# Performance work log

Hardware: AMD Instinct MI355X
Metric: run time of the kernel (lower is better)

Reference implementation:

```python
import jax, jax.numpy as jnp
import numpy as np

EPS = 1e-5

def _conv1x1(x, w, b):
    # x: [B, Cin, L], w: [Cout, Cin], b: [Cout]
    return jnp.einsum('oc,bcl->bol', w, x) + b[None, :, None]

def _bn(x, g, b):
    # BatchNorm1d in training mode: batch stats over (B, L), biased variance
    m = jnp.mean(x, axis=(0, 2), keepdims=True)
    v = jnp.var(x, axis=(0, 2), keepdims=True)
    return g[None, :, None] * (x - m) * jax.lax.rsqrt(v + EPS) + b[None, :, None]

def setup_inputs() -> dict:
    key = jax.random.key(0)
    ks = jax.random.split(key, 16)
    B, H, L, K = 32, 32, 32768, 7
    rel, im, out = H // 16, H // 8, H // 4          # 2, 4, 8
    cat = (1 + K) * rel                              # 16
    w = lambda k, shape: jax.random.normal(k, shape, jnp.float32) * 0.1
    return {
        'x': jax.random.normal(ks[0], (B, H, L), jnp.float32),
        'w_phi': w(ks[1], (rel, H)),  'b_phi': w(ks[2], (rel,)),
        'w_psi': w(ks[3], (rel, H)),  'b_psi': w(ks[4], (rel,)),
        'w_beta': w(ks[5], (out, H)), 'b_beta': w(ks[6], (out,)),
        'w_cw1': w(ks[7], (im, cat)), 'b_cw1': w(ks[8], (im,)),
        'w_cw2': w(ks[9], (out, im)), 'b_cw2': w(ks[10], (out,)),
        'w_out': w(ks[11], (H, out)), 'b_out': w(ks[12], (H,)),
        'g_cat': jnp.ones((cat,), jnp.float32),  'be_cat': jnp.zeros((cat,), jnp.float32),
        'g_im': jnp.ones((im,), jnp.float32),    'be_im': jnp.zeros((im,), jnp.float32),
        'g_aggr': jnp.ones((out,), jnp.float32), 'be_aggr': jnp.zeros((out,), jnp.float32),
        'g_hid': jnp.ones((H,), jnp.float32),    'be_hid': jnp.zeros((H,), jnp.float32),
        'kernel_size': 7,
    }

def reference(x, w_phi, b_phi, w_psi, b_psi, w_beta, b_beta,
              w_cw1, b_cw1, w_cw2, b_cw2, w_out, b_out,
              g_cat, be_cat, g_im, be_im, g_aggr, be_aggr, g_hid, be_hid,
              kernel_size):
    B, H, L = x.shape
    phi = _conv1x1(x, w_phi, b_phi)                       # [B, rel, L]
    psi = _conv1x1(x, w_psi, b_psi)                       # [B, rel, L]
    p = kernel_size // 2
    psi_pad = jnp.pad(psi, ((0, 0), (0, 0), (p, p)))
    # F.unfold with kernel (k,1): channel index = c*k + j -> stack kernel axis after channel
    psi_unf = jnp.stack([psi_pad[:, :, j:j + L] for j in range(kernel_size)], axis=2)
    psi_unf = psi_unf.reshape(B, psi.shape[1] * kernel_size, L)   # [B, rel*k, L]
    h = jnp.concatenate([phi, psi_unf], axis=1)           # [B, (1+k)*rel, L]
    h = jax.nn.relu(_bn(h, g_cat, be_cat))
    h = _conv1x1(h, w_cw1, b_cw1)
    h = jax.nn.relu(_bn(h, g_im, be_im))
    weight = _conv1x1(h, w_cw2, b_cw2)                    # [B, out, L]
    beta = _conv1x1(x, w_beta, b_beta)                    # [B, out, L]
    aggr = jax.nn.relu(_bn(weight * beta, g_aggr, be_aggr))
    y = x + _conv1x1(aggr, w_out, b_out)
    return jax.nn.relu(_bn(y, g_hid, be_hid))
```

## Files before the change

### kernel.cpp

```cpp
#include <hip/hip_runtime.h>
#include <math.h>

#define Bn 32
#define Hc 32
#define Ln 32768
#define RELC 2
#define IMC 4
#define OC 8
#define CATC 16
#define KS 7
#define NPOS (Bn*Ln)
#define TPB 256
#define VPT 4
#define PPB (TPB*VPT)
#define TILES (Ln/PPB)
#define NBLK (Bn*TILES)
#define NSLOT 16
#define SSTR 128

#define iS_PHI  0
#define iSS_PHI 2
#define iS_PSI  4
#define iSS_PSI 6
#define iS_T    8
#define iSS_T   12
#define iS_AP   16
#define iSS_AP  24
#define iS_Y    32
#define iSS_Y   64
#define bPF  0
#define bPFS 6
#define bQL  12
#define bQLS 18
#define NBST 24

#define FMA4(A,S,V) { A.x=fmaf((S),(V).x,A.x); A.y=fmaf((S),(V).y,A.y); A.z=fmaf((S),(V).z,A.z); A.w=fmaf((S),(V).w,A.w); }

__device__ inline float4 affrelu(float4 v, float a, float d){
    float4 r;
    r.x=fmaxf(fmaf(a,v.x,d),0.f); r.y=fmaxf(fmaf(a,v.y,d),0.f);
    r.z=fmaxf(fmaf(a,v.z,d),0.f); r.w=fmaxf(fmaf(a,v.w,d),0.f);
    return r;
}
__device__ inline double wredd(double v){
    #pragma unroll
    for (int o=32;o>0;o>>=1) v += __shfl_down(v,o,64);
    return v;
}
__device__ inline float wredf(float v){
    #pragma unroll
    for (int o=32;o>0;o>>=1) v += __shfl_down(v,o,64);
    return v;
}
__device__ inline void atomAddD(double* p, double v){ unsafeAtomicAdd(p, v); }

__device__ inline unsigned short f2b(float f){
    unsigned int u = __float_as_uint(f);
    u += 0x7FFFu + ((u>>16)&1u);
    return (unsigned short)(u>>16);
}
__device__ inline float b2f(unsigned short h){ return __uint_as_float(((unsigned int)h)<<16); }
__device__ inline ushort4 pack4r(float4 v, float4* r){
    ushort4 h;
    h.x=f2b(v.x); h.y=f2b(v.y); h.z=f2b(v.z); h.w=f2b(v.w);
    r->x=b2f(h.x); r->y=b2f(h.y); r->z=b2f(h.z); r->w=b2f(h.w);
    return h;
}
__device__ inline ushort4 pack4(float4 v){
    ushort4 h;
    h.x=f2b(v.x); h.y=f2b(v.y); h.z=f2b(v.z); h.w=f2b(v.w);
    return h;
}
__device__ inline float4 unpack4(ushort4 h){
    return make_float4(b2f(h.x),b2f(h.y),b2f(h.z),b2f(h.w));
}
typedef unsigned short us8 __attribute__((ext_vector_type(8)));
typedef float f4nt __attribute__((ext_vector_type(4)));
__device__ inline void ntstore4(float* p, float4 v){
    union { float4 a; f4nt b; } u; u.a = v;
    __builtin_nontemporal_store(u.b, (f4nt*)p);
}

template<int NCH>
__device__ void affines(const double* __restrict__ stats, const double* __restrict__ bstats,
                        const float* g_cat, const float* be_cat,
                        const float* g_im,  const float* be_im,
                        const float* g_ag,  const float* be_ag,
                        const float* g_hid, const float* be_hid,
                        double (*redS)[16], double (*redQ)[16],
                        double* bstL, float* aAll, float* dAll, int tid)
{
    if (tid < NBST) bstL[tid] = bstats[tid];
    for (int p = tid; p < NCH*16; p += TPB){
        int ch = p >> 4, s = p & 15;
        int si, qi;
        if (ch < 2)       { si = iS_PHI+ch;           qi = iSS_PHI+ch; }
        else if (ch < 16) { int cp=(ch-2)/KS;         si = iS_PSI+cp;  qi = iSS_PSI+cp; }
        else if (ch < 20) { int i=ch-16;              si = iS_T+i;     qi = iSS_T+i; }
        else if (ch < 28) { int o=ch-20;              si = iS_AP+o;    qi = iSS_AP+o; }
        else              { int h=ch-28;              si = iS_Y+h;     qi = iSS_Y+h; }
        redS[ch][s] = stats[(size_t)s*SSTR + si];
        redQ[ch][s] = stats[(size_t)s*SSTR + qi];
    }
    __syncthreads();
    if (tid < NCH){
        double S=0, SS=0;
        #pragma unroll
        for (int s=0;s<16;++s){ S += redS[tid][s]; SS += redQ[tid][s]; }
        float g, be;
        if (tid < 16){
            if (tid >= 2){
                int cp=(tid-2)/KS, j=(tid-2)%KS, d=j-KS/2;
                if (d>0) for (int i=0;i<d;++i)   { S-=bstL[bPF+cp*3+i]; SS-=bstL[bPFS+cp*3+i]; }
                if (d<0) for (int i=3+d;i<3;++i) { S-=bstL[bQL+cp*3+i]; SS-=bstL[bQLS+cp*3+i]; }
            }
            g=g_cat[tid]; be=be_cat[tid];
        } else if (tid < 20){ g=g_im[tid-16]; be=be_im[tid-16]; }
        else if (tid < 28){ g=g_ag[tid-20]; be=be_ag[tid-20]; }
        else { g=g_hid[tid-28]; be=be_hid[tid-28]; }
        const double N=(double)NPOS;
        double m=S/N, v=SS/N-m*m, inv=1.0/sqrt(v+1e-5);
        aAll[tid]=(float)(g*inv);
        dAll[tid]=be-(float)(m*inv*g);
    }
}

__global__ void __launch_bounds__(TPB) k1m(
    const float* __restrict__ x,
    const float* __restrict__ w_phi, const float* __restrict__ b_phi,
    const float* __restrict__ w_psi, const float* __restrict__ b_psi,
    const float* __restrict__ w_beta,const float* __restrict__ b_beta,
    unsigned short* __restrict__ phiB, unsigned short* __restrict__ psiB,
    unsigned short* __restrict__ betaB, unsigned short* __restrict__ xB,
    double* __restrict__ stats, double* __restrict__ bstats)
{
    __shared__ __align__(16) float wl[Hc*12 + 12];
    __shared__ double rbuf[4][8];
    const int tid = threadIdx.x;
    for (int i = tid; i < Hc*12; i += TPB) {
        int h = i/12, j = i%12;
        float v;
        if (j < 2)      v = w_phi[j*Hc + h];
        else if (j < 4) v = w_psi[(j-2)*Hc + h];
        else            v = w_beta[(j-4)*Hc + h];
        wl[h*12 + j] = v;
    }
    if (tid < 12)
        wl[Hc*12+tid] = (tid<2) ? b_phi[tid] : (tid<4) ? b_psi[tid-2] : b_beta[tid-4];
    __syncthreads();

    const int b    = blockIdx.x / TILES;
    const int tile = blockIdx.x % TILES;
    const int l0   = tile*PPB + tid*VPT;
    double* st = stats + (size_t)(blockIdx.x & (NSLOT-1))*SSTR;

    const float* xp = x + (size_t)b*Hc*Ln + l0;
    unsigned short* xw = xB + (size_t)b*Hc*Ln + l0;

    float4 accA[4];
    #pragma unroll
    for (int j=0;j<4;++j){ float bb = wl[Hc*12+j]; accA[j]=make_float4(bb,bb,bb,bb); }
    #pragma unroll 8
    for (int h=0; h<Hc; ++h) {
        const float4 xv = *(const float4*)(xp + (size_t)h*Ln);
        const float4 w0 = *(const float4*)(&wl[h*12+0]);
        FMA4(accA[0],w0.x,xv); FMA4(accA[1],w0.y,xv);
        FMA4(accA[2],w0.z,xv); FMA4(accA[3],w0.w,xv);
        *(ushort4*)(xw + (size_t)h*Ln) = pack4(xv);
    }
    float4 accB[OC];
    #pragma unroll
    for (int o=0;o<OC;++o){ float bb = wl[Hc*12+4+o]; accB[o]=make_float4(bb,bb,bb,bb); }
    #pragma unroll 8
    for (int h=0; h<Hc; ++h) {
        const float4 hv = unpack4(*(const ushort4*)(xw + (size_t)h*Ln));
        const float4 w1 = *(const float4*)(&wl[h*12+4]);
        const float4 w2 = *(const float4*)(&wl[h*12+8]);
        FMA4(accB[0],w1.x,hv); FMA4(accB[1],w1.y,hv); FMA4(accB[2],w1.z,hv); FMA4(accB[3],w1.w,hv);
        FMA4(accB[4],w2.x,hv); FMA4(accB[5],w2.y,hv); FMA4(accB[6],w2.z,hv); FMA4(accB[7],w2.w,hv);
    }

    float4 rphi[2], rpsi[2];
    #pragma unroll
    for (int c=0;c<RELC;++c){
        ushort4 hp = pack4r(accA[c], &rphi[c]);
        *(ushort4*)(phiB + ((size_t)(b*RELC+c))*Ln + l0) = hp;
        ushort4 hq = pack4r(accA[2+c], &rpsi[c]);
        *(ushort4*)(psiB + ((size_t)(b*RELC+c))*Ln + l0) = hq;
    }
    #pragma unroll
    for (int o=0;o<OC;++o)
        *(ushort4*)(betaB + ((size_t)(b*OC+o))*Ln + l0) = pack4(accB[o]);

    double vals[8];
    #pragma unroll
    for (int c=0;c<2;++c){
        float4 v = rphi[c];
        vals[c]   = (double)v.x+v.y+v.z+v.w;
        vals[2+c] = (double)v.x*v.x+(double)v.y*v.y+(double)v.z*v.z+(double)v.w*v.w;
        float4 u = rpsi[c];
        vals[4+c] = (double)u.x+u.y+u.z+u.w;
        vals[6+c] = (double)u.x*u.x+(double)u.y*u.y+(double)u.z*u.z+(double)u.w*u.w;
    }
    if (tile==0 || tile==TILES-1) {
        #pragma unroll
        for (int c=0;c<2;++c){
            const float pv[4] = {rpsi[c].x, rpsi[c].y, rpsi[c].z, rpsi[c].w};
            #pragma unroll
            for (int e=0;e<4;++e){
                int le = l0+e;
                if (le < 3) {
                    atomAddD(&bstats[bPF +c*3+le], (double)pv[e]);
                    atomAddD(&bstats[bPFS+c*3+le], (double)pv[e]*pv[e]);
                }
                if (le >= Ln-3) {
                    int i = le-(Ln-3);
                    atomAddD(&bstats[bQL +c*3+i], (double)pv[e]);
                    atomAddD(&bstats[bQLS+c*3+i], (double)pv[e]*pv[e]);
                }
            }
        }
    }
    const int lane=tid&63, wid=tid>>6;
    #pragma unroll
    for (int i=0;i<8;++i){ double r=wredd(vals[i]); if(lane==0) rbuf[wid][i]=r; }
    __syncthreads();
    if (tid<8) atomAddD(&st[iS_PHI+tid], rbuf[0][tid]+rbuf[1][tid]+rbuf[2][tid]+rbuf[3][tid]);
}

#define STAGE_PSI_V(psiT)                                                                  \
    {                                                                                      \
        int c_ = tid >> 7, k_ = tid & 127;                                                 \
        us8 v_ = *(const us8*)(psiB + ((size_t)(b*RELC+c_))*Ln + lb + 8*k_);               \
        _Pragma("unroll")                                                                  \
        for (int j_=0;j_<8;++j_) psiT[c_][3+8*k_+j_] = b2f(v_[j_]);                        \
        if (tid < 6){ int cc=tid/3, ii=tid%3;                                              \
            psiT[cc][ii] = (tile>0) ? b2f(psiB[((size_t)(b*RELC+cc))*Ln + lb-3+ii]) : 0.f; }\
        else if (tid < 12){ int kk=tid-6, cc=kk/3, ii=kk%3;                                \
            psiT[cc][1027+ii] = (tile<TILES-1) ? b2f(psiB[((size_t)(b*RELC+cc))*Ln + lb+1024+ii]) : 0.f; } \
    }

#define COMPUTE_T(tacc,aCat,dCat,w1s,b1s,psiT)                                             \
    _Pragma("unroll")                                                                      \
    for (int o=0;o<IMC;++o){ float bb=b1s[o]; tacc[o]=make_float4(bb,bb,bb,bb); }          \
    _Pragma("unroll")                                                                      \
    for (int c=0;c<RELC;++c){                                                              \
        float4 pv = unpack4(*(const ushort4*)(phiB + ((size_t)(b*RELC+c))*Ln + lb + li));  \
        float4 hv = affrelu(pv, aCat[c], dCat[c]);                                         \
        _Pragma("unroll")                                                                  \
        for (int o=0;o<IMC;++o) FMA4(tacc[o], w1s[o*CATC+c], hv);                          \
    }                                                                                      \
    _Pragma("unroll")                                                                      \
    for (int c=0;c<RELC;++c){                                                              \
        float4 A  = *(const float4*)&psiT[c][li];                                          \
        float4 Bv = *(const float4*)&psiT[c][li+4];                                        \
        float4 Cv = *(const float4*)&psiT[c][li+8];                                        \
        float pr[12] = {A.x,A.y,A.z,A.w, Bv.x,Bv.y,Bv.z,Bv.w, Cv.x,Cv.y,Cv.z,Cv.w};        \
        _Pragma("unroll")                                                                  \
        for (int j=0;j<KS;++j){                                                            \
            int ch = 2 + c*KS + j;                                                         \
            float a=aCat[ch], d=dCat[ch];                                                  \
            float4 hv;                                                                     \
            hv.x=fmaxf(fmaf(a,pr[j+0],d),0.f);                                             \
            hv.y=fmaxf(fmaf(a,pr[j+1],d),0.f);                                             \
            hv.z=fmaxf(fmaf(a,pr[j+2],d),0.f);                                             \
            hv.w=fmaxf(fmaf(a,pr[j+3],d),0.f);                                             \
            _Pragma("unroll")                                                              \
            for (int o=0;o<IMC;++o) FMA4(tacc[o], w1s[o*CATC+ch], hv);                     \
        }                                                                                  \
    }

#define COMPUTE_AG(ag,tacc,aIm,dIm,aAg,dAg,w2s,b2s)                                        \
    {                                                                                      \
        float4 h2[IMC];                                                                    \
        _Pragma("unroll")                                                                  \
        for (int i=0;i<IMC;++i) h2[i]=affrelu(tacc[i],aIm[i],dIm[i]);                      \
        _Pragma("unroll")                                                                  \
        for (int o=0;o<OC;++o){                                                            \
            float bb=b2s[o];                                                               \
            float4 w=make_float4(bb,bb,bb,bb);                                             \
            _Pragma("unroll")                                                              \
            for (int i=0;i<IMC;++i) FMA4(w,w2s[o*IMC+i],h2[i]);                            \
            float4 bv = unpack4(*(const ushort4*)(betaB + ((size_t)(b*OC+o))*Ln + lb + li)); \
            float4 av; av.x=w.x*bv.x; av.y=w.y*bv.y; av.z=w.z*bv.z; av.w=w.w*bv.w;         \
            ag[o]=affrelu(av, aAg[o], dAg[o]);                                             \
        }                                                                                  \
    }

__global__ void __launch_bounds__(TPB) k3t(
    const unsigned short* __restrict__ phiB, const unsigned short* __restrict__ psiB,
    const float* __restrict__ w_cw1, const float* __restrict__ b_cw1,
    const float* __restrict__ g_cat, const float* __restrict__ be_cat,
    double* __restrict__ stats, const double* __restrict__ bstats)
{
    __shared__ float w1s[IMC*CATC], b1s[IMC];
    __shared__ __align__(16) float psiT[2][1032];
    __shared__ double rbuf[4][8];
    __shared__ double redS[16][16], redQ[16][16];
    __shared__ double bstL[NBST];
    __shared__ float aAll[16], dAll[16];
    const int tid = threadIdx.x;
    const int b    = blockIdx.x / TILES;
    const int tile = blockIdx.x % TILES;
    const int lb   = tile*PPB;
    const int li   = tid*VPT;
    double* st = stats + (size_t)(blockIdx.x & (NSLOT-1))*SSTR;

    if (tid < IMC*CATC) w1s[tid] = w_cw1[tid];
    if (tid < IMC)      b1s[tid] = b_cw1[tid];
    STAGE_PSI_V(psiT)
    affines<16>(stats,bstats, g_cat,be_cat, 0,0, 0,0, 0,0, redS,redQ,bstL,aAll,dAll, tid);
    __syncthreads();

    float4 tacc[IMC];
    COMPUTE_T(tacc,aAll,dAll,w1s,b1s,psiT)

    double vals[8];
    #pragma unroll
    for (int o=0;o<IMC;++o){
        float4 v = tacc[o];
        vals[o]   = (double)v.x+v.y+v.z+v.w;
        vals[4+o] = (double)v.x*v.x+(double)v.y*v.y+(double)v.z*v.z+(double)v.w*v.w;
    }
    const int lane=tid&63, wid=tid>>6;
    #pragma unroll
    for (int i=0;i<8;++i){ double r=wredd(vals[i]); if(lane==0) rbuf[wid][i]=r; }
    __syncthreads();
    if (tid<8) atomAddD(&st[iS_T+tid], rbuf[0][tid]+rbuf[1][tid]+rbuf[2][tid]+rbuf[3][tid]);
}

__global__ void __launch_bounds__(TPB) k5a(
    const unsigned short* __restrict__ phiB, const unsigned short* __restrict__ psiB,
    const unsigned short* __restrict__ betaB,
    const float* __restrict__ w_cw1, const float* __restrict__ b_cw1,
    const float* __restrict__ w_cw2, const float* __restrict__ b_cw2,
    const float* __restrict__ g_cat, const float* __restrict__ be_cat,
    const float* __restrict__ g_im,  const float* __restrict__ be_im,
    double* __restrict__ stats, const double* __restrict__ bstats)
{
    __shared__ float w1s[IMC*CATC], b1s[IMC], w2s[OC*IMC], b2s[OC];
    __shared__ __align__(16) float psiT[2][1032];
    __shared__ double rbuf[4][16];
    __shared__ double redS[20][16], redQ[20][16];
    __shared__ double bstL[NBST];
    __shared__ float aAll[20], dAll[20];
    const int tid = threadIdx.x;
    const int b    = blockIdx.x / TILES;
    const int tile = blockIdx.x % TILES;
    const int lb   = tile*PPB;
    const int li   = tid*VPT;
    double* st = stats + (size_t)(blockIdx.x & (NSLOT-1))*SSTR;

    if (tid < IMC*CATC) w1s[tid] = w_cw1[tid];
    if (tid < IMC)      b1s[tid] = b_cw1[tid];
    if (tid>=64 && tid<64+OC*IMC) w2s[tid-64]=w_cw2[tid-64];
    if (tid>=96 && tid<96+OC)     b2s[tid-96]=b_cw2[tid-96];
    STAGE_PSI_V(psiT)
    affines<20>(stats,bstats, g_cat,be_cat, g_im,be_im, 0,0, 0,0, redS,redQ,bstL,aAll,dAll, tid);
    __syncthreads();

    float4 tacc[IMC];
    COMPUTE_T(tacc,aAll,dAll,w1s,b1s,psiT)

    double vals[16];
    {
        float4 h2[IMC];
        #pragma unroll
        for (int i=0;i<IMC;++i) h2[i]=affrelu(tacc[i],aAll[16+i],dAll[16+i]);
        #pragma unroll
        for (int o=0;o<OC;++o){
            float bb=b2s[o];
            float4 w=make_float4(bb,bb,bb,bb);
            #pragma unroll
            for (int i=0;i<IMC;++i) FMA4(w,w2s[o*IMC+i],h2[i]);
            float4 bv = unpack4(*(const ushort4*)(betaB + ((size_t)(b*OC+o))*Ln + lb + li));
            float4 av; av.x=w.x*bv.x; av.y=w.y*bv.y; av.z=w.z*bv.z; av.w=w.w*bv.w;
            vals[o]   = (double)av.x+av.y+av.z+av.w;
            vals[8+o] = (double)av.x*av.x+(double)av.y*av.y+(double)av.z*av.z+(double)av.w*av.w;
        }
    }
    const int lane=tid&63, wid=tid>>6;
    #pragma unroll
    for (int i=0;i<16;++i){ double r=wredd(vals[i]); if(lane==0) rbuf[wid][i]=r; }
    __syncthreads();
    if (tid<16) atomAddD(&st[iS_AP+tid], rbuf[0][tid]+rbuf[1][tid]+rbuf[2][tid]+rbuf[3][tid]);
}

__global__ void __launch_bounds__(TPB) k7y(
    const unsigned short* __restrict__ xB,
    const unsigned short* __restrict__ phiB, const unsigned short* __restrict__ psiB,
    const unsigned short* __restrict__ betaB,
    const float* __restrict__ w_cw1, const float* __restrict__ b_cw1,
    const float* __restrict__ w_cw2, const float* __restrict__ b_cw2,
    const float* __restrict__ w_out, const float* __restrict__ b_out,
    const float* __restrict__ g_cat, const float* __restrict__ be_cat,
    const float* __restrict__ g_im,  const float* __restrict__ be_im,
    const float* __restrict__ g_ag,  const float* __restrict__ be_ag,
    double* __restrict__ stats, const double* __restrict__ bstats)
{
    __shared__ float w1s[IMC*CATC], b1s[IMC], w2s[OC*IMC], b2s[OC];
    __shared__ __align__(16) float wos[Hc*OC];
    __shared__ float bos[Hc];
    __shared__ __align__(16) float psiT[2][1032];
    __shared__ float fredS[Hc][4], fredQ[Hc][4];
    __shared__ double redS[28][16], redQ[28][16];
    __shared__ double bstL[NBST];
    __shared__ float aAll[28], dAll[28];
    const int tid = threadIdx.x;
    const int b    = blockIdx.x / TILES;
    const int tile = blockIdx.x % TILES;
    const int lb   = tile*PPB;
    const int li   = tid*VPT;
    double* st = stats + (size_t)(blockIdx.x & (NSLOT-1))*SSTR;

    if (tid < IMC*CATC) w1s[tid] = w_cw1[tid];
    if (tid < IMC)      b1s[tid] = b_cw1[tid];
    if (tid>=64 && tid<64+OC*IMC) w2s[tid-64]=w_cw2[tid-64];
    if (tid>=96 && tid<96+OC)     b2s[tid-96]=b_cw2[tid-96];
    wos[tid] = w_out[tid];
    if (tid>=128 && tid<128+Hc) bos[tid-128]=b_out[tid-128];
    STAGE_PSI_V(psiT)
    affines<28>(stats,bstats, g_cat,be_cat, g_im,be_im, g_ag,be_ag, 0,0,
                redS,redQ,bstL,aAll,dAll, tid);
    __syncthreads();

    float4 tacc[IMC];
    COMPUTE_T(tacc,aAll,dAll,w1s,b1s,psiT)
    float4 ag[OC];
    COMPUTE_AG(ag,tacc,(aAll+16),(dAll+16),(aAll+20),(dAll+20),w2s,b2s)

    const int lane=tid&63, wid=tid>>6;
    const unsigned short* xb = xB + (size_t)b*Hc*Ln + lb + li;
    #pragma unroll 8
    for (int h=0;h<Hc;++h){
        float4 y = unpack4(*(const ushort4*)(xb + (size_t)h*Ln));
        float bb=bos[h]; y.x+=bb; y.y+=bb; y.z+=bb; y.w+=bb;
        #pragma unroll
        for (int o=0;o<OC;++o) FMA4(y, wos[h*OC+o], ag[o]);
        float fs=y.x+y.y+y.z+y.w;
        float fq=y.x*y.x+y.y*y.y+y.z*y.z+y.w*y.w;
        fs=wredf(fs); fq=wredf(fq);
        if (lane==0){ fredS[h][wid]=fs; fredQ[h][wid]=fq; }
    }
    __syncthreads();
    if (tid<Hc){
        double s=(double)fredS[tid][0]+fredS[tid][1]+fredS[tid][2]+fredS[tid][3];
        double q=(double)fredQ[tid][0]+fredQ[tid][1]+fredQ[tid][2]+fredQ[tid][3];
        atomAddD(&st[iS_Y +tid], s);
        atomAddD(&st[iSS_Y+tid], q);
    }
}

__global__ void __launch_bounds__(TPB) k9o(
    const unsigned short* __restrict__ xB,
    const unsigned short* __restrict__ phiB, const unsigned short* __restrict__ psiB,
    const unsigned short* __restrict__ betaB,
    const float* __restrict__ w_cw1, const float* __restrict__ b_cw1,
    const float* __restrict__ w_cw2, const float* __restrict__ b_cw2,
    const float* __restrict__ w_out, const float* __restrict__ b_out,
    const float* __restrict__ g_cat, const float* __restrict__ be_cat,
    const float* __restrict__ g_im,  const float* __restrict__ be_im,
    const float* __restrict__ g_ag,  const float* __restrict__ be_ag,
    const float* __restrict__ g_hid, const float* __restrict__ be_hid,
    float* __restrict__ out,
    const double* __restrict__ stats, const double* __restrict__ bstats)
{
    __shared__ float w1s[IMC*CATC], b1s[IMC], w2s[OC*IMC], b2s[OC];
    __shared__ __align__(16) float wos[Hc*OC];
    __shared__ float bos[Hc];
    __shared__ __align__(16) float psiT[2][1032];
    __shared__ double redS[60][16], redQ[60][16];
    __shared__ double bstL[NBST];
    __shared__ float aAll[60], dAll[60];
    const int tid = threadIdx.x;
    const int b    = blockIdx.x / TILES;
    const int tile = blockIdx.x % TILES;
    const int lb   = tile*PPB;
    const int li   = tid*VPT;

    if (tid < IMC*CATC) w1s[tid] = w_cw1[tid];
    if (tid < IMC)      b1s[tid] = b_cw1[tid];
    if (tid>=64 && tid<64+OC*IMC) w2s[tid-64]=w_cw2[tid-64];
    if (tid>=96 && tid<96+OC)     b2s[tid-96]=b_cw2[tid-96];
    wos[tid] = w_out[tid];
    if (tid>=128 && tid<128+Hc) bos[tid-128]=b_out[tid-128];
    STAGE_PSI_V(psiT)
    affines<60>(stats,bstats, g_cat,be_cat, g_im,be_im, g_ag,be_ag, g_hid,be_hid,
                redS,redQ,bstL,aAll,dAll, tid);
    __syncthreads();

    float4 tacc[IMC];
    COMPUTE_T(tacc,aAll,dAll,w1s,b1s,psiT)
    float4 ag[OC];
    COMPUTE_AG(ag,tacc,(aAll+16),(dAll+16),(aAll+20),(dAll+20),w2s,b2s)

    const unsigned short* xb = xB + (size_t)b*Hc*Ln + lb + li;
    float* ob = out + (size_t)b*Hc*Ln + lb + li;
    #pragma unroll 8
    for (int h=0;h<Hc;++h){
        float4 y = unpack4(*(const ushort4*)(xb + (size_t)h*Ln));
        float bb=bos[h]; y.x+=bb; y.y+=bb; y.z+=bb; y.w+=bb;
        #pragma unroll
        for (int o=0;o<OC;++o) FMA4(y, wos[h*OC+o], ag[o]);
        ntstore4(ob + (size_t)h*Ln, affrelu(y, aAll[28+h], dAll[28+h]));
    }
}

extern "C" void kernel_launch(void* const* d_in, const int* in_sizes, int n_in,
                              void* d_out, int out_size, void* d_ws, size_t ws_size,
                              hipStream_t stream)
{
    const float* x     =(const float*)d_in[0];
    const float* w_phi =(const float*)d_in[1];  const float* b_phi =(const float*)d_in[2];
    const float* w_psi =(const float*)d_in[3];  const float* b_psi =(const float*)d_in[4];
    const float* w_beta=(const float*)d_in[5];  const float* b_beta=(const float*)d_in[6];
    const float* w_cw1 =(const float*)d_in[7];  const float* b_cw1 =(const float*)d_in[8];
    const float* w_cw2 =(const float*)d_in[9];  const float* b_cw2 =(const float*)d_in[10];
    const float* w_out =(const float*)d_in[11]; const float* b_out =(const float*)d_in[12];
    const float* g_cat =(const float*)d_in[13]; const float* be_cat=(const float*)d_in[14];
    const float* g_im  =(const float*)d_in[15]; const float* be_im =(const float*)d_in[16];
    const float* g_ag  =(const float*)d_in[17]; const float* be_ag =(const float*)d_in[18];
    const float* g_hid =(const float*)d_in[19]; const float* be_hid=(const float*)d_in[20];

    double* stats  = (double*)d_ws;
    double* bstats = stats + (size_t)NSLOT*SSTR;
    unsigned short* base = (unsigned short*)((char*)d_ws + 32768);
    unsigned short* phiB  = base;
    unsigned short* psiB  = phiB  + (size_t)Bn*RELC*Ln;
    unsigned short* betaB = psiB  + (size_t)Bn*RELC*Ln;
    unsigned short* xB    = betaB + (size_t)Bn*OC*Ln;

    hipMemsetAsync(d_ws, 0, ((size_t)NSLOT*SSTR + NBST)*sizeof(double), stream);
    k1m<<<NBLK, TPB, 0, stream>>>(x, w_phi,b_phi, w_psi,b_psi, w_beta,b_beta,
                                  phiB,psiB,betaB,xB, stats,bstats);
    k3t<<<NBLK, TPB, 0, stream>>>(phiB,psiB, w_cw1,b_cw1, g_cat,be_cat, stats,bstats);
    k5a<<<NBLK, TPB, 0, stream>>>(phiB,psiB,betaB, w_cw1,b_cw1, w_cw2,b_cw2,
                                  g_cat,be_cat, g_im,be_im, stats,bstats);
    k7y<<<NBLK, TPB, 0, stream>>>(xB, phiB,psiB,betaB, w_cw1,b_cw1, w_cw2,b_cw2, w_out,b_out,
                                  g_cat,be_cat, g_im,be_im, g_ag,be_ag, stats,bstats);
    k9o<<<NBLK, TPB, 0, stream>>>(xB, phiB,psiB,betaB, w_cw1,b_cw1, w_cw2,b_cw2, w_out,b_out,
                                  g_cat,be_cat, g_im,be_im, g_ag,be_ag, g_hid,be_hid,
                                  (float*)d_out, stats,bstats);
}
```

Baseline: 173.6 us.

## Split x conversion into row kernel, pad rows, and materialize aggr for row-wise final pass

```diff
diff --git a/kernel.cpp b/kernel.cpp
--- a/kernel.cpp
+++ b/kernel.cpp
@@ -4,6 +4,7 @@
 #define Bn 32
 #define Hc 32
 #define Ln 32768
+#define RS (Ln+64)
 #define RELC 2
 #define IMC 4
 #define OC 8
@@ -125,13 +126,22 @@
     }
 }
 
-__global__ void __launch_bounds__(TPB) k1m(
-    const float* __restrict__ x,
+__global__ void __launch_bounds__(TPB) k0(const float* __restrict__ x, unsigned short* __restrict__ xB)
+{
+    const int r = blockIdx.x;
+    const float* src = x + (size_t)r*Ln;
+    unsigned short* dst = xB + (size_t)r*RS;
+    for (int i = threadIdx.x; i < Ln/4; i += TPB)
+        ((ushort4*)dst)[i] = pack4(((const float4*)src)[i]);
+}
+
+__global__ void __launch_bounds__(TPB) k1c(
+    const unsigned short* __restrict__ xB,
     const float* __restrict__ w_phi, const float* __restrict__ b_phi,
     const float* __restrict__ w_psi, const float* __restrict__ b_psi,
     const float* __restrict__ w_beta,const float* __restrict__ b_beta,
     unsigned short* __restrict__ phiB, unsigned short* __restrict__ psiB,
-    unsigned short* __restrict__ betaB, unsigned short* __restrict__ xB,
+    unsigned short* __restrict__ betaB,
     double* __restrict__ stats, double* __restrict__ bstats)
 {
     __shared__ __align__(16) float wl[Hc*12 + 12];
@@ -154,43 +164,32 @@
     const int l0   = tile*PPB + tid*VPT;
     double* st = stats + (size_t)(blockIdx.x & (NSLOT-1))*SSTR;
 
-    const float* xp = x + (size_t)b*Hc*Ln + l0;
-    unsigned short* xw = xB + (size_t)b*Hc*Ln + l0;
-
-    float4 accA[4];
-    #pragma unroll
-    for (int j=0;j<4;++j){ float bb = wl[Hc*12+j]; accA[j]=make_float4(bb,bb,bb,bb); }
+    float4 acc[12];
+    #pragma unroll
+    for (int j=0;j<12;++j){ float bb = wl[Hc*12+j]; acc[j]=make_float4(bb,bb,bb,bb); }
+
+    const unsigned short* xb = xB + (size_t)b*Hc*RS + l0;
     #pragma unroll 8
     for (int h=0; h<Hc; ++h) {
-        const float4 xv = *(const float4*)(xp + (size_t)h*Ln);
+        const float4 xv = unpack4(*(const ushort4*)(xb + (size_t)h*RS));
         const float4 w0 = *(const float4*)(&wl[h*12+0]);
-        FMA4(accA[0],w0.x,xv); FMA4(accA[1],w0.y,xv);
-        FMA4(accA[2],w0.z,xv); FMA4(accA[3],w0.w,xv);
-        *(ushort4*)(xw + (size_t)h*Ln) = pack4(xv);
-    }
-    float4 accB[OC];
-    #pragma unroll
-    for (int o=0;o<OC;++o){ float bb = wl[Hc*12+4+o]; accB[o]=make_float4(bb,bb,bb,bb); }
-    #pragma unroll 8
-    for (int h=0; h<Hc; ++h) {
-        const float4 hv = unpack4(*(const ushort4*)(xw + (size_t)h*Ln));
         const float4 w1 = *(const float4*)(&wl[h*12+4]);
         const float4 w2 = *(const float4*)(&wl[h*12+8]);
-        FMA4(accB[0],w1.x,hv); FMA4(accB[1],w1.y,hv); FMA4(accB[2],w1.z,hv); FMA4(accB[3],w1.w,hv);
-        FMA4(accB[4],w2.x,hv); FMA4(accB[5],w2.y,hv); FMA4(accB[6],w2.z,hv); FMA4(accB[7],w2.w,hv);
-    }
-
+        FMA4(acc[0],w0.x,xv); FMA4(acc[1],w0.y,xv); FMA4(acc[2],w0.z,xv); FMA4(acc[3],w0.w,xv);
+        FMA4(acc[4],w1.x,xv); FMA4(acc[5],w1.y,xv); FMA4(acc[6],w1.z,xv); FMA4(acc[7],w1.w,xv);
+        FMA4(acc[8],w2.x,xv); FMA4(acc[9],w2.y,xv); FMA4(acc[10],w2.z,xv); FMA4(acc[11],w2.w,xv);
+    }
     float4 rphi[2], rpsi[2];
     #pragma unroll
     for (int c=0;c<RELC;++c){
-        ushort4 hp = pack4r(accA[c], &rphi[c]);
-        *(ushort4*)(phiB + ((size_t)(b*RELC+c))*Ln + l0) = hp;
-        ushort4 hq = pack4r(accA[2+c], &rpsi[c]);
-        *(ushort4*)(psiB + ((size_t)(b*RELC+c))*Ln + l0) = hq;
+        ushort4 hp = pack4r(acc[c], &rphi[c]);
+        *(ushort4*)(phiB + ((size_t)(b*RELC+c))*RS + l0) = hp;
+        ushort4 hq = pack4r(acc[2+c], &rpsi[c]);
+        *(ushort4*)(psiB + ((size_t)(b*RELC+c))*RS + l0) = hq;
     }
     #pragma unroll
     for (int o=0;o<OC;++o)
-        *(ushort4*)(betaB + ((size_t)(b*OC+o))*Ln + l0) = pack4(accB[o]);
+        *(ushort4*)(betaB + ((size_t)(b*OC+o))*RS + l0) = pack4(acc[4+o]);
 
     double vals[8];
     #pragma unroll
@@ -231,13 +230,13 @@
 #define STAGE_PSI_V(psiT)                                                                  \
     {                                                                                      \
         int c_ = tid >> 7, k_ = tid & 127;                                                 \
-        us8 v_ = *(const us8*)(psiB + ((size_t)(b*RELC+c_))*Ln + lb + 8*k_);               \
+        us8 v_ = *(const us8*)(psiB + ((size_t)(b*RELC+c_))*RS + lb + 8*k_);               \
         _Pragma("unroll")                                                                  \
         for (int j_=0;j_<8;++j_) psiT[c_][3+8*k_+j_] = b2f(v_[j_]);                        \
         if (tid < 6){ int cc=tid/3, ii=tid%3;                                              \
-            psiT[cc][ii] = (tile>0) ? b2f(psiB[((size_t)(b*RELC+cc))*Ln + lb-3+ii]) : 0.f; }\
+            psiT[cc][ii] = (tile>0) ? b2f(psiB[((size_t)(b*RELC+cc))*RS + lb-3+ii]) : 0.f; }\
         else if (tid < 12){ int kk=tid-6, cc=kk/3, ii=kk%3;                                \
-            psiT[cc][1027+ii] = (tile<TILES-1) ? b2f(psiB[((size_t)(b*RELC+cc))*Ln + lb+1024+ii]) : 0.f; } \
+            psiT[cc][1027+ii] = (tile<TILES-1) ? b2f(psiB[((size_t)(b*RELC+cc))*RS + lb+1024+ii]) : 0.f; } \
     }
 
 #define COMPUTE_T(tacc,aCat,dCat,w1s,b1s,psiT)                                             \
@@ -245,7 +244,7 @@
     for (int o=0;o<IMC;++o){ float bb=b1s[o]; tacc[o]=make_float4(bb,bb,bb,bb); }          \
     _Pragma("unroll")                                                                      \
     for (int c=0;c<RELC;++c){                                                              \
-        float4 pv = unpack4(*(const ushort4*)(phiB + ((size_t)(b*RELC+c))*Ln + lb + li));  \
+        float4 pv = unpack4(*(const ushort4*)(phiB + ((size_t)(b*RELC+c))*RS + lb + li));  \
         float4 hv = affrelu(pv, aCat[c], dCat[c]);                                         \
         _Pragma("unroll")                                                                  \
         for (int o=0;o<IMC;++o) FMA4(tacc[o], w1s[o*CATC+c], hv);                          \
@@ -281,7 +280,7 @@
             float4 w=make_float4(bb,bb,bb,bb);                                             \
             _Pragma("unroll")                                                              \
             for (int i=0;i<IMC;++i) FMA4(w,w2s[o*IMC+i],h2[i]);                            \
-            float4 bv = unpack4(*(const ushort4*)(betaB + ((size_t)(b*OC+o))*Ln + lb + li)); \
+            float4 bv = unpack4(*(const ushort4*)(betaB + ((size_t)(b*OC+o))*RS + lb + li)); \
             float4 av; av.x=w.x*bv.x; av.y=w.y*bv.y; av.z=w.z*bv.z; av.w=w.w*bv.w;         \
             ag[o]=affrelu(av, aAg[o], dAg[o]);                                             \
         }                                                                                  \
@@ -373,7 +372,7 @@
             float4 w=make_float4(bb,bb,bb,bb);
             #pragma unroll
             for (int i=0;i<IMC;++i) FMA4(w,w2s[o*IMC+i],h2[i]);
-            float4 bv = unpack4(*(const ushort4*)(betaB + ((size_t)(b*OC+o))*Ln + lb + li));
+            float4 bv = unpack4(*(const ushort4*)(betaB + ((size_t)(b*OC+o))*RS + lb + li));
             float4 av; av.x=w.x*bv.x; av.y=w.y*bv.y; av.z=w.z*bv.z; av.w=w.w*bv.w;
             vals[o]   = (double)av.x+av.y+av.z+av.w;
             vals[8+o] = (double)av.x*av.x+(double)av.y*av.y+(double)av.z*av.z+(double)av.w*av.w;
@@ -386,10 +385,11 @@
     if (tid<16) atomAddD(&st[iS_AP+tid], rbuf[0][tid]+rbuf[1][tid]+rbuf[2][tid]+rbuf[3][tid]);
 }
 
+template<int WAG>
 __global__ void __launch_bounds__(TPB) k7y(
     const unsigned short* __restrict__ xB,
     const unsigned short* __restrict__ phiB, const unsigned short* __restrict__ psiB,
-    const unsigned short* __restrict__ betaB,
+    const unsigned short* __restrict__ betaB, unsigned short* __restrict__ agB,
     const float* __restrict__ w_cw1, const float* __restrict__ b_cw1,
     const float* __restrict__ w_cw2, const float* __restrict__ b_cw2,
     const float* __restrict__ w_out, const float* __restrict__ b_out,
@@ -428,12 +428,19 @@
     COMPUTE_T(tacc,aAll,dAll,w1s,b1s,psiT)
     float4 ag[OC];
     COMPUTE_AG(ag,tacc,(aAll+16),(dAll+16),(aAll+20),(dAll+20),w2s,b2s)
+    if (WAG){
+        #pragma unroll
+        for (int o=0;o<OC;++o){
+            ushort4 hh = pack4r(ag[o], &ag[o]);
+            *(ushort4*)(agB + ((size_t)(b*OC+o))*RS + lb + li) = hh;
+        }
+    }
 
     const int lane=tid&63, wid=tid>>6;
-    const unsigned short* xb = xB + (size_t)b*Hc*Ln + lb + li;
+    const unsigned short* xb = xB + (size_t)b*Hc*RS + lb + li;
     #pragma unroll 8
     for (int h=0;h<Hc;++h){
-        float4 y = unpack4(*(const ushort4*)(xb + (size_t)h*Ln));
+        float4 y = unpack4(*(const ushort4*)(xb + (size_t)h*RS));
         float bb=bos[h]; y.x+=bb; y.y+=bb; y.z+=bb; y.w+=bb;
         #pragma unroll
         for (int o=0;o<OC;++o) FMA4(y, wos[h*OC+o], ag[o]);
@@ -494,15 +501,75 @@
     float4 ag[OC];
     COMPUTE_AG(ag,tacc,(aAll+16),(dAll+16),(aAll+20),(dAll+20),w2s,b2s)
 
-    const unsigned short* xb = xB + (size_t)b*Hc*Ln + lb + li;
+    const unsigned short* xb = xB + (size_t)b*Hc*RS + lb + li;
     float* ob = out + (size_t)b*Hc*Ln + lb + li;
     #pragma unroll 8
     for (int h=0;h<Hc;++h){
-        float4 y = unpack4(*(const ushort4*)(xb + (size_t)h*Ln));
+        float4 y = unpack4(*(const ushort4*)(xb + (size_t)h*RS));
         float bb=bos[h]; y.x+=bb; y.y+=bb; y.z+=bb; y.w+=bb;
         #pragma unroll
         for (int o=0;o<OC;++o) FMA4(y, wos[h*OC+o], ag[o]);
         ntstore4(ob + (size_t)h*Ln, affrelu(y, aAll[28+h], dAll[28+h]));
+    }
+}
+
+__global__ void __launch_bounds__(TPB) k9oT(
+    const unsigned short* __restrict__ xB, const unsigned short* __restrict__ agB,
+    const float* __restrict__ w_out, const float* __restrict__ b_out,
+    const float* __restrict__ g_hid, const float* __restrict__ be_hid,
+    float* __restrict__ out, const double* __restrict__ stats)
+{
+    __shared__ double redS[Hc][16], redQ[Hc][16];
+    __shared__ float aH[Hc], dH[Hc], wos8[OC];
+    __shared__ float bias;
+    const int tid = threadIdx.x;
+    const int r = blockIdx.x;
+    const int b = r >> 5, h = r & 31;
+
+    for (int p = tid; p < Hc*16; p += TPB){
+        int ch = p >> 4, s = p & 15;
+        redS[ch][s] = stats[(size_t)s*SSTR + iS_Y + ch];
+        redQ[ch][s] = stats[(size_t)s*SSTR + iSS_Y + ch];
+    }
+    if (tid < OC) wos8[tid] = w_out[h*OC + tid];
+    if (tid == OC) bias = b_out[h];
+    __syncthreads();
+    if (tid < Hc){
+        double S=0, SS=0;
+        #pragma unroll
+        for (int s=0;s<16;++s){ S += redS[tid][s]; SS += redQ[tid][s]; }
+        const double N=(double)NPOS;
+        double m=S/N, v=SS/N-m*m, inv=1.0/sqrt(v+1e-5);
+        aH[tid]=(float)(g_hid[tid]*inv);
+        dH[tid]=be_hid[tid]-(float)(m*inv*g_hid[tid]);
+    }
+    __syncthreads();
+    const float a = aH[h], d = dH[h], bb = bias;
+    float w8[OC];
+    #pragma unroll
+    for (int o=0;o<OC;++o) w8[o]=wos8[o];
+
+    const us8* xr = (const us8*)(xB + (size_t)r*RS);
+    float* orow = out + (size_t)r*Ln;
+    for (int i = tid; i < Ln/8; i += TPB){
+        us8 xv = xr[i];
+        float y[8];
+        #pragma unroll
+        for (int j=0;j<8;++j) y[j] = b2f(xv[j]) + bb;
+        #pragma unroll
+        for (int o=0;o<OC;++o){
+            us8 av = *(const us8*)(agB + (size_t)(b*OC+o)*RS + 8*i);
+            float w = w8[o];
+            #pragma unroll
+            for (int j=0;j<8;++j) y[j] = fmaf(w, b2f(av[j]), y[j]);
+        }
+        float4 o0, o1;
+        o0.x=fmaxf(fmaf(a,y[0],d),0.f); o0.y=fmaxf(fmaf(a,y[1],d),0.f);
+        o0.z=fmaxf(fmaf(a,y[2],d),0.f); o0.w=fmaxf(fmaf(a,y[3],d),0.f);
+        o1.x=fmaxf(fmaf(a,y[4],d),0.f); o1.y=fmaxf(fmaf(a,y[5],d),0.f);
+        o1.z=fmaxf(fmaf(a,y[6],d),0.f); o1.w=fmaxf(fmaf(a,y[7],d),0.f);
+        ntstore4(orow + 8*i,     o0);
+        ntstore4(orow + 8*i + 4, o1);
     }
 }
 
@@ -526,19 +593,33 @@
     double* bstats = stats + (size_t)NSLOT*SSTR;
     unsigned short* base = (unsigned short*)((char*)d_ws + 32768);
     unsigned short* phiB  = base;
-    unsigned short* psiB  = phiB  + (size_t)Bn*RELC*Ln;
-    unsigned short* betaB = psiB  + (size_t)Bn*RELC*Ln;
-    unsigned short* xB    = betaB + (size_t)Bn*OC*Ln;
+    unsigned short* psiB  = phiB  + (size_t)64*RS;
+    unsigned short* betaB = psiB  + (size_t)64*RS;
+    unsigned short* xB    = betaB + (size_t)256*RS;
+    unsigned short* agB   = xB    + (size_t)1024*RS;
+
+    const size_t need_ag = 32768 + (size_t)(64+64+256+1024+256)*RS*sizeof(unsigned short);
+    const bool useAg = (ws_size >= need_ag);
 
     hipMemsetAsync(d_ws, 0, ((size_t)NSLOT*SSTR + NBST)*sizeof(double), stream);
-    k1m<<<NBLK, TPB, 0, stream>>>(x, w_phi,b_phi, w_psi,b_psi, w_beta,b_beta,
-                                  phiB,psiB,betaB,xB, stats,bstats);
+    k0 <<<Bn*Hc, TPB, 0, stream>>>(x, xB);
+    k1c<<<NBLK, TPB, 0, stream>>>(xB, w_phi,b_phi, w_psi,b_psi, w_beta,b_beta,
+                                  phiB,psiB,betaB, stats,bstats);
     k3t<<<NBLK, TPB, 0, stream>>>(phiB,psiB, w_cw1,b_cw1, g_cat,be_cat, stats,bstats);
     k5a<<<NBLK, TPB, 0, stream>>>(phiB,psiB,betaB, w_cw1,b_cw1, w_cw2,b_cw2,
                                   g_cat,be_cat, g_im,be_im, stats,bstats);
-    k7y<<<NBLK, TPB, 0, stream>>>(xB, phiB,psiB,betaB, w_cw1,b_cw1, w_cw2,b_cw2, w_out,b_out,
-                                  g_cat,be_cat, g_im,be_im, g_ag,be_ag, stats,bstats);
-    k9o<<<NBLK, TPB, 0, stream>>>(xB, phiB,psiB,betaB, w_cw1,b_cw1, w_cw2,b_cw2, w_out,b_out,
-                                  g_cat,be_cat, g_im,be_im, g_ag,be_ag, g_hid,be_hid,
-                                  (float*)d_out, stats,bstats);
-}
+    if (useAg){
+        k7y<1><<<NBLK, TPB, 0, stream>>>(xB, phiB,psiB,betaB, agB, w_cw1,b_cw1, w_cw2,b_cw2,
+                                         w_out,b_out, g_cat,be_cat, g_im,be_im, g_ag,be_ag,
+                                         stats,bstats);
+        k9oT<<<Bn*Hc, TPB, 0, stream>>>(xB, agB, w_out,b_out, g_hid,be_hid,
+                                        (float*)d_out, stats);
+    } else {
+        k7y<0><<<NBLK, TPB, 0, stream>>>(xB, phiB,psiB,betaB, agB, w_cw1,b_cw1, w_cw2,b_cw2,
+                                         w_out,b_out, g_cat,be_cat, g_im,be_im, g_ag,be_ag,
+                                         stats,bstats);
+        k9o<<<NBLK, TPB, 0, stream>>>(xB, phiB,psiB,betaB, w_cw1,b_cw1, w_cw2,b_cw2,
+                                      w_out,b_out, g_cat,be_cat, g_im,be_im, g_ag,be_ag,
+                                      g_hid,be_hid, (float*)d_out, stats,bstats);
+    }
+}
```

Result: slower. 185.3 us (+6.8%).
